# Performance work log

Hardware: AMD Instinct MI355X
Metric: run time of the kernel (lower is better)

Reference implementation:

```python
import jax, jax.numpy as jnp
import numpy as np

N = 524288          # number of query points
L_FREQ = 16         # frequencies in positional encoding -> dim_encoding = 3*2*16 = 96
DIM_ENC = 96
DIM_HID = 128
NUM_LAYERS = 8      # 1 input layer + 7 hidden layers + 1 output layer
DIM_OUT = 4
DIM_IN_HID = DIM_HID + DIM_ENC  # concat skip: 224


def setup_inputs() -> dict:
    key = jax.random.key(0)
    ks = jax.random.split(key, 7)
    def lin(k, fan_in, shape):
        return jax.random.uniform(k, shape, jnp.float32, -1.0, 1.0) / np.sqrt(fan_in)
    return {
        "query_points": jax.random.uniform(ks[0], (N, 3), jnp.float32),
        "W0": lin(ks[1], DIM_ENC, (DIM_ENC, DIM_HID)),
        "b0": lin(ks[2], DIM_ENC, (DIM_HID,)),
        "Wh": lin(ks[3], DIM_IN_HID, (NUM_LAYERS - 1, DIM_IN_HID, DIM_HID)),
        "bh": lin(ks[4], DIM_IN_HID, (NUM_LAYERS - 1, DIM_HID)),
        "Wl": lin(ks[5], DIM_IN_HID, (DIM_IN_HID, DIM_OUT)),
        "bl": lin(ks[6], DIM_IN_HID, (DIM_OUT,)),
    }


def _encode(x):
    # NeRF frequency encoding: [N,3] -> [N, 3*2*L_FREQ]
    freqs = (2.0 ** jnp.arange(L_FREQ, dtype=x.dtype)) * jnp.pi
    xf = x[..., None] * freqs                      # [N, 3, L]
    enc = jnp.concatenate([jnp.sin(xf), jnp.cos(xf)], axis=-1)  # [N, 3, 2L]
    return enc.reshape(x.shape[0], -1)             # [N, 96]


def reference(query_points, W0, b0, Wh, bh, Wl, bl):
    enc = _encode(query_points)                    # [N, 96]
    outs = jnp.maximum(enc @ W0 + b0, 0.0)         # [N, 128]
    outs = jnp.concatenate([outs, enc], axis=-1)   # concat skip -> [N, 224]
    for i in range(Wh.shape[0]):                   # 7 structurally-distinct hidden layers
        outs = jnp.maximum(outs @ Wh[i] + bh[i], 0.0)
        outs = jnp.concatenate([outs, enc], axis=-1)
    return outs @ Wl + bl                          # [N, 4], no activation on last layer
```

## Files before the change

### kernel.cpp

```cpp
#include <hip/hip_runtime.h>
#include <stdint.h>

typedef unsigned short u16;
typedef __bf16 bf16x8 __attribute__((ext_vector_type(8)));
typedef float f32x4 __attribute__((ext_vector_type(4)));
typedef float f32x16 __attribute__((ext_vector_type(16)));
typedef unsigned int u32;

#define IMG_H(l) (14336 + ((l)-1) * 30720)
#define IMG_OUT 229376
#define IMG_TOTAL 237056

__device__ inline int fmap(int k) {
    int s = k >> 4, h = (k >> 3) & 1, j = k & 7;
    return 32 * (s >> 1) + 16 * (s & 1) + 8 * (j >> 2) + 4 * h + (j & 3);
}
__device__ inline u16 b16rne(float v) {
    u32 u = __builtin_bit_cast(u32, v);
    u += 0x7FFFu + ((u >> 16) & 1u);
    return (u16)(u >> 16);
}

__global__ void nf_prep(const float* __restrict__ W0, const float* __restrict__ b0,
                        const float* __restrict__ Wh, const float* __restrict__ bh,
                        const float* __restrict__ Wl, const float* __restrict__ bl,
                        u16* __restrict__ img) {
    int idx = blockIdx.x * 256 + threadIdx.x;
    if (idx >= IMG_TOTAL) return;
    float v;
    if (idx < 14336) {
        int gg = idx >> 3, j = idx & 7;
        int koct = gg >> 7, i = gg & 127, k = koct * 8 + j;
        v = (k < 96) ? W0[k * 128 + i] : (k == 96) ? b0[i] : 0.f;
    } else if (idx < IMG_OUT) {
        int r = idx - 14336, l = r / 30720, rr = r % 30720;
        int gg = rr >> 3, j = rr & 7;
        int koct = gg >> 7, i = gg & 127, k = koct * 8 + j;
        const float* W = Wh + l * 224 * 128;
        v = (k < 128) ? W[fmap(k) * 128 + i]
          : (k < 224) ? W[k * 128 + i]
          : (k == 224) ? bh[l * 128 + i] : 0.f;
    } else {
        int r = idx - IMG_OUT;
        int gg = r >> 3, j = r & 7;
        int koct = gg >> 5, i = gg & 31, k = koct * 8 + j;
        v = 0.f;
        if (i < 4)
            v = (k < 128) ? Wl[fmap(k) * 4 + i]
              : (k < 224) ? Wl[k * 4 + i]
              : (k == 224) ? bl[i] : 0.f;
    }
    img[idx & 7 ? idx : idx] = 0;
    img[idx] = b16rne(v);
}

__device__ inline f32x16 MF32(bf16x8 a, bf16x8 b, f32x16 c) {
    return __builtin_amdgcn_mfma_f32_32x32x16_bf16(a, b, c, 0, 0, 0);
}
__device__ inline bf16x8 fr4(const u32 (&p)[4]) {
    union { u32 u[4]; bf16x8 v; } x;
    x.u[0] = p[0]; x.u[1] = p[1]; x.u[2] = p[2]; x.u[3] = p[3];
    return x.v;
}
__device__ inline bf16x8 frCB(u32 c0) {
    union { u32 u[4]; bf16x8 v; } x;
    x.u[0] = c0; x.u[1] = 0; x.u[2] = 0; x.u[3] = 0;
    return x.v;
}
__device__ inline bf16x8 ldA(const u16* base, int gi) {
    union { uint4 q; bf16x8 v; } x;
    x.q = *(const uint4*)(base + (gi << 3));
    return x.v;
}
__device__ inline u32 pkbf(float a, float b) {
    u32 ua = __builtin_bit_cast(u32, a) + 0x8000u;
    u32 ub = __builtin_bit_cast(u32, b) + 0x8000u;
    return __builtin_amdgcn_perm(ub, ua, 0x07060302u);
}
__device__ inline void stageA(const u16* gsrc, u16* ldst, int bytes, int wave, int lane) {
    const char* gs = (const char*)gsrc + lane * 16;
    char* ls = (char*)ldst;
    for (int c = wave * 1024; c < bytes; c += 4096)
        __builtin_amdgcn_global_load_lds(
            (const __attribute__((address_space(1))) void*)(gs + c),
            (__attribute__((address_space(3))) void*)(ls + c), 16, 0, 0);
}
__device__ inline void zeroacc(f32x16 (&acc)[4][2]) {
#pragma unroll
    for (int t = 0; t < 4; t++)
#pragma unroll
        for (int n = 0; n < 2; n++)
#pragma unroll
            for (int r = 0; r < 16; r++) acc[t][n][r] = 0.f;
}
__device__ inline void buildH(const f32x16 (&acc)[4][2], u32 (&H)[2][8][4]) {
#pragma unroll
    for (int n = 0; n < 2; n++)
#pragma unroll
        for (int s = 0; s < 8; s++) {
            const int t = s >> 1, rb = (s & 1) * 8;
#pragma unroll
            for (int q = 0; q < 4; q++)
                H[n][s][q] = pkbf(fmaxf(acc[t][n][rb + 2 * q], 0.f),
                                  fmaxf(acc[t][n][rb + 2 * q + 1], 0.f));
        }
}
__device__ inline void cHid0(const u16* A, int h, int m32, f32x16 (&acc)[4][2],
                             const u32 (&H)[2][8][4]) {
#pragma unroll
    for (int s = 0; s < 8; s++) {
        bf16x8 B0 = fr4(H[0][s]), B1 = fr4(H[1][s]);
#pragma unroll
        for (int t = 0; t < 4; t++) {
            bf16x8 a = ldA(A, (2 * s + h) * 128 + t * 32 + m32);
            acc[t][0] = MF32(a, B0, acc[t][0]);
            acc[t][1] = MF32(a, B1, acc[t][1]);
        }
    }
}
__device__ inline void cHid1(const u16* A, int h, int m32, f32x16 (&acc)[4][2],
                             const u32 (&E)[2][3][2][4], u32 CB0) {
#pragma unroll
    for (int s = 0; s < 7; s++) {
        bf16x8 B0, B1;
        if (s < 6) { B0 = fr4(E[0][s >> 1][s & 1]); B1 = fr4(E[1][s >> 1][s & 1]); }
        else       { B0 = frCB(CB0); B1 = B0; }
#pragma unroll
        for (int t = 0; t < 4; t++) {
            bf16x8 a = ldA(A, (2 * s + h) * 128 + t * 32 + m32);
            acc[t][0] = MF32(a, B0, acc[t][0]);
            acc[t][1] = MF32(a, B1, acc[t][1]);
        }
    }
}

__global__ __launch_bounds__(256, 2) void nf_main(const float* __restrict__ qp,
                                                  const u16* __restrict__ img,
                                                  float* __restrict__ out) {
    __shared__ alignas(16) u16 lds[2][16384];
    const int tid = threadIdx.x, wave = tid >> 6, lane = tid & 63;
    const int m32 = lane & 31, h = lane >> 5;
    const int pbase = blockIdx.x * 256 + wave * 64;

    stageA(img, &lds[0][0], 16384, wave, lane);

    u32 E[2][3][2][4];
    const float sc0 = h ? 128.0f : 0.5f;
#pragma unroll
    for (int n = 0; n < 2; n++)
#pragma unroll
        for (int c = 0; c < 3; c++) {
            float r = qp[(pbase + n * 32 + m32) * 3 + c] * sc0;
            float sn[8], cs[8];
#pragma unroll
            for (int t = 0; t < 8; t++) {
                float fr = __builtin_amdgcn_fractf(r);
                sn[t] = __builtin_amdgcn_sinf(fr);
                cs[t] = __builtin_amdgcn_cosf(fr);
                r = r * 2.0f;
            }
#pragma unroll
            for (int q = 0; q < 4; q++) {
                E[n][c][0][q] = pkbf(sn[2 * q], sn[2 * q + 1]);
                E[n][c][1][q] = pkbf(cs[2 * q], cs[2 * q + 1]);
            }
        }
    const u32 CB0 = (h == 0) ? 0x00003F80u : 0u;

    f32x16 acc[4][2];
    u32 H[2][8][4];
    zeroacc(acc);

    __syncthreads();
    stageA(img + 8192, &lds[1][0], 12288, wave, lane);
#pragma unroll
    for (int s = 0; s < 4; s++) {
        bf16x8 B0 = fr4(E[0][s >> 1][s & 1]), B1 = fr4(E[1][s >> 1][s & 1]);
#pragma unroll
        for (int t = 0; t < 4; t++) {
            bf16x8 a = ldA(&lds[0][0], (2 * s + h) * 128 + t * 32 + m32);
            acc[t][0] = MF32(a, B0, acc[t][0]);
            acc[t][1] = MF32(a, B1, acc[t][1]);
        }
    }
    __syncthreads();
    stageA(img + IMG_H(1), &lds[0][0], 32768, wave, lane);
#pragma unroll
    for (int s = 0; s < 3; s++) {
        bf16x8 B0, B1;
        if (s < 2) { B0 = fr4(E[0][2][s]); B1 = fr4(E[1][2][s]); }
        else       { B0 = frCB(CB0); B1 = B0; }
#pragma unroll
        for (int t = 0; t < 4; t++) {
            bf16x8 a = ldA(&lds[1][0], (2 * s + h) * 128 + t * 32 + m32);
            acc[t][0] = MF32(a, B0, acc[t][0]);
            acc[t][1] = MF32(a, B1, acc[t][1]);
        }
    }
    buildH(acc, H);
    __syncthreads();

#pragma unroll 1
    for (int l = 1; l < 8; l++) {
        const int base = IMG_H(l);
        stageA(img + base + 16384, &lds[1][0], 28672, wave, lane);
        zeroacc(acc);
        cHid0(&lds[0][0], h, m32, acc, H);
        __syncthreads();
        const u16* nsrc = (l < 7) ? (img + base + 30720) : (img + IMG_OUT);
        stageA(nsrc, &lds[0][0], (l < 7) ? 32768 : 15360, wave, lane);
        cHid1(&lds[1][0], h, m32, acc, E, CB0);
        buildH(acc, H);
        __syncthreads();
    }

    f32x16 o0, o1;
#pragma unroll
    for (int r = 0; r < 16; r++) { o0[r] = 0.f; o1[r] = 0.f; }
#pragma unroll
    for (int s = 0; s < 15; s++) {
        bf16x8 B0, B1;
        if (s < 8)       { B0 = fr4(H[0][s]); B1 = fr4(H[1][s]); }
        else if (s < 14) { B0 = fr4(E[0][(s - 8) >> 1][(s - 8) & 1]);
                           B1 = fr4(E[1][(s - 8) >> 1][(s - 8) & 1]); }
        else             { B0 = frCB(CB0); B1 = B0; }
        bf16x8 a = ldA(&lds[0][0], (2 * s + h) * 32 + m32);
        o0 = MF32(a, B0, o0);
        o1 = MF32(a, B1, o1);
    }
    if (h == 0) {
        f32x4 w0 = {o0[0], o0[1], o0[2], o0[3]};
        f32x4 w1 = {o1[0], o1[1], o1[2], o1[3]};
        *(f32x4*)(out + 4 * (pbase + m32)) = w0;
        *(f32x4*)(out + 4 * (pbase + 32 + m32)) = w1;
    }
}

extern "C" void kernel_launch(void* const* d_in, const int* in_sizes, int n_in,
                              void* d_out, int out_size, void* d_ws, size_t ws_size,
                              hipStream_t stream) {
    const float* qp = (const float*)d_in[0];
    const float* W0 = (const float*)d_in[1];
    const float* b0 = (const float*)d_in[2];
    const float* Wh = (const float*)d_in[3];
    const float* bh = (const float*)d_in[4];
    const float* Wl = (const float*)d_in[5];
    const float* bl = (const float*)d_in[6];
    float* out = (float*)d_out;
    u16* img = (u16*)d_ws;

    nf_prep<<<926, 256, 0, stream>>>(W0, b0, Wh, bh, Wl, bl, img);
    nf_main<<<2048, 256, 0, stream>>>(qp, img, out);
}
```

Baseline: 269.3 us.

## Triple-buffer weight staging in LDS with fine-grained vmcnt waits and priority

Replaces the two-buffer LDS scheme with three smaller buffers, so each layer's weights are streamed in three chunks and the next chunk's global loads overlap the current chunk's MFMAs. The __syncthreads calls become explicit s_waitcnt vmcnt counts plus raw barriers, so only the needed loads are waited on. MFMA sections are wrapped in s_setprio to favour math waves. The hand-tuned vmcnt counts are fragile: if they do not match stageA's actual load count, reads can race with pending loads. A redundant store in the prep kernel is also removed.

```diff
diff --git a/kernel.cpp b/kernel.cpp
--- a/kernel.cpp
+++ b/kernel.cpp
@@ -50,7 +50,6 @@
               : (k < 224) ? Wl[k * 4 + i]
               : (k == 224) ? bl[i] : 0.f;
     }
-    img[idx & 7 ? idx : idx] = 0;
     img[idx] = b16rne(v);
 }
 
@@ -105,44 +104,74 @@
                                   fmaxf(acc[t][n][rb + 2 * q + 1], 0.f));
         }
 }
-__device__ inline void cHid0(const u16* A, int h, int m32, f32x16 (&acc)[4][2],
-                             const u32 (&H)[2][8][4]) {
-#pragma unroll
-    for (int s = 0; s < 8; s++) {
-        bf16x8 B0 = fr4(H[0][s]), B1 = fr4(H[1][s]);
-#pragma unroll
-        for (int t = 0; t < 4; t++) {
-            bf16x8 a = ldA(A, (2 * s + h) * 128 + t * 32 + m32);
-            acc[t][0] = MF32(a, B0, acc[t][0]);
-            acc[t][1] = MF32(a, B1, acc[t][1]);
-        }
-    }
-}
-__device__ inline void cHid1(const u16* A, int h, int m32, f32x16 (&acc)[4][2],
+
+#define WAITV(N) asm volatile("s_waitcnt vmcnt(" #N ")" ::: "memory")
+#define BAR() do { __builtin_amdgcn_s_barrier(); __builtin_amdgcn_sched_barrier(0); } while (0)
+
+__device__ inline void mmRow(const u16* A, int h, int m32, int s,
+                             bf16x8 B0, bf16x8 B1, f32x16 (&acc)[4][2]) {
+#pragma unroll
+    for (int t = 0; t < 4; t++) {
+        bf16x8 a = ldA(A, (2 * s + h) * 128 + t * 32 + m32);
+        acc[t][0] = MF32(a, B0, acc[t][0]);
+        acc[t][1] = MF32(a, B1, acc[t][1]);
+    }
+}
+
+__device__ inline void cH04(const u16* A, int h, int m32, f32x16 (&acc)[4][2],
+                            const u32 (&H)[2][8][4]) {
+    __builtin_amdgcn_s_setprio(1);
+#pragma unroll
+    for (int s = 0; s < 5; s++)
+        mmRow(A, h, m32, s, fr4(H[0][s]), fr4(H[1][s]), acc);
+    __builtin_amdgcn_s_setprio(0);
+}
+__device__ inline void cH57E0(const u16* A, int h, int m32, f32x16 (&acc)[4][2],
+                              const u32 (&H)[2][8][4], const u32 (&E)[2][3][2][4]) {
+    __builtin_amdgcn_s_setprio(1);
+    mmRow(A, h, m32, 0, fr4(H[0][5]), fr4(H[1][5]), acc);
+    mmRow(A, h, m32, 1, fr4(H[0][6]), fr4(H[1][6]), acc);
+    mmRow(A, h, m32, 2, fr4(H[0][7]), fr4(H[1][7]), acc);
+    mmRow(A, h, m32, 3, fr4(E[0][0][0]), fr4(E[1][0][0]), acc);
+    mmRow(A, h, m32, 4, fr4(E[0][0][1]), fr4(E[1][0][1]), acc);
+    __builtin_amdgcn_s_setprio(0);
+}
+__device__ inline void cE12b(const u16* A, int h, int m32, f32x16 (&acc)[4][2],
                              const u32 (&E)[2][3][2][4], u32 CB0) {
-#pragma unroll
-    for (int s = 0; s < 7; s++) {
-        bf16x8 B0, B1;
-        if (s < 6) { B0 = fr4(E[0][s >> 1][s & 1]); B1 = fr4(E[1][s >> 1][s & 1]); }
-        else       { B0 = frCB(CB0); B1 = B0; }
-#pragma unroll
-        for (int t = 0; t < 4; t++) {
-            bf16x8 a = ldA(A, (2 * s + h) * 128 + t * 32 + m32);
-            acc[t][0] = MF32(a, B0, acc[t][0]);
-            acc[t][1] = MF32(a, B1, acc[t][1]);
-        }
-    }
+    __builtin_amdgcn_s_setprio(1);
+    mmRow(A, h, m32, 0, fr4(E[0][1][0]), fr4(E[1][1][0]), acc);
+    mmRow(A, h, m32, 1, fr4(E[0][1][1]), fr4(E[1][1][1]), acc);
+    mmRow(A, h, m32, 2, fr4(E[0][2][0]), fr4(E[1][2][0]), acc);
+    mmRow(A, h, m32, 3, fr4(E[0][2][1]), fr4(E[1][2][1]), acc);
+    mmRow(A, h, m32, 4, frCB(CB0), frCB(CB0), acc);
+    __builtin_amdgcn_s_setprio(0);
+}
+__device__ inline void cL0a(const u16* A, int h, int m32, f32x16 (&acc)[4][2],
+                            const u32 (&E)[2][3][2][4]) {
+    __builtin_amdgcn_s_setprio(1);
+#pragma unroll
+    for (int s = 0; s < 5; s++)
+        mmRow(A, h, m32, s, fr4(E[0][s >> 1][s & 1]), fr4(E[1][s >> 1][s & 1]), acc);
+    __builtin_amdgcn_s_setprio(0);
+}
+__device__ inline void cL0b(const u16* A, int h, int m32, f32x16 (&acc)[4][2],
+                            const u32 (&E)[2][3][2][4], u32 CB0) {
+    __builtin_amdgcn_s_setprio(1);
+    mmRow(A, h, m32, 0, fr4(E[0][2][1]), fr4(E[1][2][1]), acc);
+    mmRow(A, h, m32, 1, frCB(CB0), frCB(CB0), acc);
+    __builtin_amdgcn_s_setprio(0);
 }
 
 __global__ __launch_bounds__(256, 2) void nf_main(const float* __restrict__ qp,
                                                   const u16* __restrict__ img,
                                                   float* __restrict__ out) {
-    __shared__ alignas(16) u16 lds[2][16384];
+    __shared__ alignas(16) u16 lds[3][10240];
     const int tid = threadIdx.x, wave = tid >> 6, lane = tid & 63;
     const int m32 = lane & 31, h = lane >> 5;
     const int pbase = blockIdx.x * 256 + wave * 64;
 
-    stageA(img, &lds[0][0], 16384, wave, lane);
+    stageA(img, &lds[0][0], 20480, wave, lane);
+    stageA(img + 10240, &lds[1][0], 8192, wave, lane);
 
     u32 E[2][3][2][4];
     const float sc0 = h ? 128.0f : 0.5f;
@@ -171,52 +200,39 @@
     u32 H[2][8][4];
     zeroacc(acc);
 
-    __syncthreads();
-    stageA(img + 8192, &lds[1][0], 12288, wave, lane);
-#pragma unroll
-    for (int s = 0; s < 4; s++) {
-        bf16x8 B0 = fr4(E[0][s >> 1][s & 1]), B1 = fr4(E[1][s >> 1][s & 1]);
-#pragma unroll
-        for (int t = 0; t < 4; t++) {
-            bf16x8 a = ldA(&lds[0][0], (2 * s + h) * 128 + t * 32 + m32);
-            acc[t][0] = MF32(a, B0, acc[t][0]);
-            acc[t][1] = MF32(a, B1, acc[t][1]);
-        }
-    }
-    __syncthreads();
-    stageA(img + IMG_H(1), &lds[0][0], 32768, wave, lane);
-#pragma unroll
-    for (int s = 0; s < 3; s++) {
-        bf16x8 B0, B1;
-        if (s < 2) { B0 = fr4(E[0][2][s]); B1 = fr4(E[1][2][s]); }
-        else       { B0 = frCB(CB0); B1 = B0; }
-#pragma unroll
-        for (int t = 0; t < 4; t++) {
-            bf16x8 a = ldA(&lds[1][0], (2 * s + h) * 128 + t * 32 + m32);
-            acc[t][0] = MF32(a, B0, acc[t][0]);
-            acc[t][1] = MF32(a, B1, acc[t][1]);
-        }
-    }
+    WAITV(2); BAR();
+    stageA(img + IMG_H(1), &lds[2][0], 20480, wave, lane);
+    cL0a(&lds[0][0], h, m32, acc, E);
+    WAITV(5); BAR();
+    stageA(img + IMG_H(1) + 10240, &lds[0][0], 20480, wave, lane);
+    cL0b(&lds[1][0], h, m32, acc, E, CB0);
     buildH(acc, H);
-    __syncthreads();
+    WAITV(5); BAR();
 
 #pragma unroll 1
     for (int l = 1; l < 8; l++) {
         const int base = IMG_H(l);
-        stageA(img + base + 16384, &lds[1][0], 28672, wave, lane);
+        stageA(img + base + 20480, &lds[1][0], 20480, wave, lane);
         zeroacc(acc);
-        cHid0(&lds[0][0], h, m32, acc, H);
-        __syncthreads();
-        const u16* nsrc = (l < 7) ? (img + base + 30720) : (img + IMG_OUT);
-        stageA(nsrc, &lds[0][0], (l < 7) ? 32768 : 15360, wave, lane);
-        cHid1(&lds[1][0], h, m32, acc, E, CB0);
+        cH04(&lds[2][0], h, m32, acc, H);
+        WAITV(5); BAR();
+        const u16* nsrc = (l < 7) ? (img + IMG_H(l + 1)) : (img + IMG_OUT);
+        stageA(nsrc, &lds[2][0], (l < 7) ? 20480 : 15360, wave, lane);
+        cH57E0(&lds[0][0], h, m32, acc, H, E);
+        if (l < 7) { WAITV(5); } else { WAITV(3); }
+        BAR();
+        if (l < 7)
+            stageA(img + IMG_H(l + 1) + 10240, &lds[0][0], 20480, wave, lane);
+        cE12b(&lds[1][0], h, m32, acc, E, CB0);
         buildH(acc, H);
-        __syncthreads();
+        if (l < 7) { WAITV(5); } else { WAITV(0); }
+        BAR();
     }
 
     f32x16 o0, o1;
 #pragma unroll
     for (int r = 0; r < 16; r++) { o0[r] = 0.f; o1[r] = 0.f; }
+    __builtin_amdgcn_s_setprio(1);
 #pragma unroll
     for (int s = 0; s < 15; s++) {
         bf16x8 B0, B1;
@@ -224,10 +240,11 @@
         else if (s < 14) { B0 = fr4(E[0][(s - 8) >> 1][(s - 8) & 1]);
                            B1 = fr4(E[1][(s - 8) >> 1][(s - 8) & 1]); }
         else             { B0 = frCB(CB0); B1 = B0; }
-        bf16x8 a = ldA(&lds[0][0], (2 * s + h) * 32 + m32);
+        bf16x8 a = ldA(&lds[2][0], (2 * s + h) * 32 + m32);
         o0 = MF32(a, B0, o0);
         o1 = MF32(a, B1, o1);
     }
+    __builtin_amdgcn_s_setprio(0);
     if (h == 0) {
         f32x4 w0 = {o0[0], o0[1], o0[2], o0[3]};
         f32x4 w1 = {o1[0], o1[1], o1[2], o1[3]};
```

Result: faster. 261.7 us (-2.8%).
